# Optimization experiments

Measured on AMD Instinct MI355X. Metric: run time of the kernel, lower is better.

Reference implementation:

```python
import jax, jax.numpy as jnp
import numpy as np

N, E, DIM, H = 100000, 1600000, 128, 8
HD = DIM // H


def setup_inputs() -> dict:
    key = jax.random.key(0)
    ks = jax.random.split(key, 12)
    inp = {
        'x': jax.random.normal(ks[0], (N, DIM), dtype=jnp.float32),
        'src': jax.random.randint(ks[1], (E,), 0, N, dtype=jnp.int32),
        'dst': jax.random.randint(ks[2], (E,), 0, N, dtype=jnp.int32),
    }
    scale = 1.0 / np.sqrt(DIM)
    for i, nm in enumerate(['q', 'k', 'v', 'o']):
        inp['W' + nm] = jax.random.normal(ks[3 + 2 * i], (DIM, DIM), dtype=jnp.float32) * scale
        inp['b' + nm] = jax.random.normal(ks[4 + 2 * i], (DIM,), dtype=jnp.float32) * 0.01
    return inp


def reference(x, src, dst, Wq, bq, Wk, bk, Wv, bv, Wo, bo):
    n = x.shape[0]
    q = (x @ Wq + bq).reshape(n, H, HD)
    k = (x @ Wk + bk).reshape(n, H, HD)
    v = (x @ Wv + bv).reshape(n, H, HD)
    # per-edge score: dot(q[src], k[dst]) over head_dim  -> [E, H]
    scores = jnp.einsum('ehd,ehd->eh', q[src], k[dst]) / np.sqrt(HD).astype(np.float32)
    # edge softmax grouped by destination node
    m = jax.ops.segment_max(scores, dst, num_segments=n)        # [N, H]
    e = jnp.exp(scores - m[dst])                                 # [E, H]
    z = jax.ops.segment_sum(e, dst, num_segments=n)              # [N, H]
    attn = e / z[dst]                                            # [E, H]
    # weighted scatter-sum of source values into destinations
    agg = jax.ops.segment_sum(v[src] * attn[:, :, None], dst, num_segments=n)  # [N, H, HD]
    out = agg.reshape(n, DIM) @ Wo + bo
    return out
```

## Files before the change

### kernel.cpp

```cpp
#include <hip/hip_runtime.h>
#include <hip/hip_bf16.h>
#include <math.h>


#define CAP 64
#define CUR_STRIDE 16
#define BCHUNK 4096

typedef __attribute__((ext_vector_type(8))) short short8;
typedef __attribute__((ext_vector_type(4))) float f32x4;

__device__ inline unsigned short f2bf(float f) {
    unsigned u = __float_as_uint(f);
    unsigned r = u + 0x7fffu + ((u >> 16) & 1u);
    return (unsigned short)(r >> 16);
}
__device__ inline float bfhi2f(unsigned u) { return __uint_as_float(u & 0xffff0000u); }
__device__ inline float bflo2f(unsigned u) { return __uint_as_float(u << 16); }

__device__ inline float w_perm(const float* Wq, const float* Wk, const float* Wv,
                               int k, int c) {
    if (c < 256) {
        int g = c >> 2, r = c & 3;
        return (r < 2) ? Wq[k * 128 + 2 * g + r] : Wv[k * 128 + 2 * g + (r - 2)];
    }
    return Wk[k * 128 + (c - 256)];
}

__global__ void pack_b_kernel(const float* __restrict__ Wq, const float* __restrict__ Wk,
                              const float* __restrict__ Wv, const float* __restrict__ Wo,
                              const float* __restrict__ bq, const float* __restrict__ bk,
                              const float* __restrict__ bv,
                              short* __restrict__ BqkvP, short* __restrict__ BoP,
                              float* __restrict__ bqkv) {
    int t = blockIdx.x * 256 + threadIdx.x;
    if (t < 24 * 4 * 64 * 8) {
        int j = t & 7, l = (t >> 3) & 63, ks = (t >> 9) & 3, ct = t >> 11;
        int c = ct * 16 + (l & 15);
        int k = ks * 32 + (l >> 4) * 8 + j;
        BqkvP[t] = (short)f2bf(w_perm(Wq, Wk, Wv, k, c));
    }
    if (t < 8 * 4 * 64 * 8) {
        int j = t & 7, l = (t >> 3) & 63, ks = (t >> 9) & 3, ct = t >> 11;
        int c = ct * 16 + (l & 15);
        int k = ks * 32 + (l >> 4) * 8 + j;
        BoP[t] = (short)f2bf(Wo[k * 128 + c]);
    }
    if (t < 384) {
        float v;
        if (t < 256) {
            int g = t >> 2, r = t & 3;
            v = (r < 2) ? bq[2 * g + r] : bv[2 * g + (r - 2)];
        } else v = bk[t - 256];
        bqkv[t] = v;
    }
}

#define QKV_STRIDE 392
__global__ __launch_bounds__(256) void gemm_qkv_mfma(const float* __restrict__ A,
        const short* __restrict__ Bp, const float* __restrict__ bias,
        short* __restrict__ qv, short* __restrict__ kb, int M) {
    __shared__ short stage[4][16][QKV_STRIDE];
    int w = threadIdx.x >> 6, l = threadIdx.x & 63;
    int row0 = blockIdx.x * 64 + w * 16;
    int lr = l & 15, lk = l >> 4;

    f32x4 acc[24];
    #pragma unroll
    for (int ct = 0; ct < 24; ++ct) {
        float b = bias[ct * 16 + lr];
        acc[ct][0] = b; acc[ct][1] = b; acc[ct][2] = b; acc[ct][3] = b;
    }

    int arow = row0 + lr;
    bool rowok = arow < M;
    const float* arp = A + (size_t)arow * 128;

    #pragma unroll
    for (int ks = 0; ks < 4; ++ks) {
        f32x4 a0 = {0.f, 0.f, 0.f, 0.f}, a1 = {0.f, 0.f, 0.f, 0.f};
        if (rowok) {
            a0 = *(const f32x4*)(arp + ks * 32 + lk * 8);
            a1 = *(const f32x4*)(arp + ks * 32 + lk * 8 + 4);
        }
        short8 af;
        af[0] = (short)f2bf(a0[0]); af[1] = (short)f2bf(a0[1]);
        af[2] = (short)f2bf(a0[2]); af[3] = (short)f2bf(a0[3]);
        af[4] = (short)f2bf(a1[0]); af[5] = (short)f2bf(a1[1]);
        af[6] = (short)f2bf(a1[2]); af[7] = (short)f2bf(a1[3]);
        #pragma unroll
        for (int ct = 0; ct < 24; ++ct) {
            short8 bf = *(const short8*)(Bp + ((size_t)(ct * 4 + ks) * 64 + l) * 8);
            acc[ct] = __builtin_amdgcn_mfma_f32_16x16x32_bf16(af, bf, acc[ct], 0, 0, 0);
        }
    }

    #pragma unroll
    for (int ct = 0; ct < 24; ++ct) {
        int c = ct * 16 + lr;
        #pragma unroll
        for (int j = 0; j < 4; ++j)
            stage[w][lk * 4 + j][c] = (short)f2bf(acc[ct][j]);
    }
    __syncthreads();

    #pragma unroll
    for (int it = 0; it < 8; ++it) {
        int rr = it * 2 + (l >> 5);
        int row = row0 + rr;
        if (row < M) {
            short8 vqv = *(const short8*)&stage[w][rr][(l & 31) * 8];
            *(short8*)(qv + (size_t)row * 256 + (l & 31) * 8) = vqv;
        }
    }
    #pragma unroll
    for (int it = 0; it < 4; ++it) {
        int rr = it * 4 + (l >> 4);
        int row = row0 + rr;
        if (row < M) {
            short8 vk = *(const short8*)&stage[w][rr][256 + (l & 15) * 8];
            *(short8*)(kb + (size_t)row * 128 + (l & 15) * 8) = vk;
        }
    }
}

__global__ __launch_bounds__(256) void build_kernel(const int* __restrict__ src,
        const int* __restrict__ dst, int* __restrict__ cursor, int* __restrict__ csr,
        int E, int per8) {
    int xcd = blockIdx.x & 7;
    int chunk = blockIdx.x >> 3;
    int lo = xcd * per8, hi = lo + per8;
    int base = chunk * BCHUNK;
    #pragma unroll
    for (int it = 0; it < BCHUNK / 256; ++it) {
        int e = base + it * 256 + threadIdx.x;
        if (e < E) {
            int d = __builtin_nontemporal_load(dst + e);
            int s = __builtin_nontemporal_load(src + e);
            if (d >= lo && d < hi) {
                int slot = atomicAdd(&cursor[d << 4], 1);
                if (slot < CAP) csr[((size_t)d << 6) + slot] = s;
            }
        }
    }
}

#define EDGE_BODY(ss)                                                          \
    {                                                                          \
        uint2 u = *(const uint2*)(qv + (size_t)(ss) * 256 + l * 4);            \
        float p = bflo2f(u.x) * kdx + bfhi2f(u.x) * kdy;                       \
        p += __shfl_xor(p, 1);                                                 \
        p += __shfl_xor(p, 2);                                                 \
        p += __shfl_xor(p, 4);                                                 \
        float e = __expf(p * 0.25f);                                           \
        z += e;                                                                \
        ax += e * bflo2f(u.y);                                                 \
        ay += e * bfhi2f(u.y);                                                 \
    }

#define AGG_STRIDE 68
__global__ __launch_bounds__(256) void edge_out_kernel(const short* __restrict__ qv,
        const short* __restrict__ kb, const int* __restrict__ cursor,
        const int* __restrict__ csr, const short* __restrict__ BoP,
        const float* __restrict__ bo, float* __restrict__ out, int N, int per8) {
    __shared__ unsigned aggLds[16][AGG_STRIDE];
    int w  = threadIdx.x >> 6;
    int l  = threadIdx.x & 63;
    int lr = l & 15, lk = l >> 4;
    int xcd = blockIdx.x & 7;
    int jb  = blockIdx.x >> 3;
    int sliceN = per8 < (N - xcd * per8) ? per8 : (N - xcd * per8);
    int local0 = jb * 16;

    #pragma unroll
    for (int q = 0; q < 4; ++q) {
        int i = w * 4 + q;
        int local = local0 + i;
        if (local < sliceN) {
            int d = xcd * per8 + local;
            int deg = cursor[d << 4];
            int n = (deg < CAP) ? deg : CAP;
            const int* ep = csr + ((size_t)d << 6);
            unsigned kpk = __builtin_nontemporal_load(
                (const unsigned*)(kb + (size_t)d * 128 + 2 * l));
            float kdx = bflo2f(kpk), kdy = bfhi2f(kpk);

            float z = 0.f, ax = 0.f, ay = 0.f;
            int ii = 0;
            for (; ii + 4 <= n; ii += 4) {
                int s0 = ep[ii];
                int s1 = ep[ii + 1];
                int s2 = ep[ii + 2];
                int s3 = ep[ii + 3];
                EDGE_BODY(s0)
                EDGE_BODY(s1)
                EDGE_BODY(s2)
                EDGE_BODY(s3)
            }
            for (; ii < n; ++ii) {
                int s0 = ep[ii];
                EDGE_BODY(s0)
            }

            float zi = (z > 0.f) ? 1.0f / z : 0.f;
            aggLds[i][l] = (unsigned)f2bf(ax * zi) | ((unsigned)f2bf(ay * zi) << 16);
        }
    }
    __syncthreads();

    f32x4 acc[2];
    #pragma unroll
    for (int t = 0; t < 2; ++t) {
        float b = bo[(w * 2 + t) * 16 + lr];
        acc[t][0] = b; acc[t][1] = b; acc[t][2] = b; acc[t][3] = b;
    }

    #pragma unroll
    for (int ks = 0; ks < 4; ++ks) {
        short8 af = *(const short8*)&aggLds[lr][ks * 16 + lk * 4];
        #pragma unroll
        for (int t = 0; t < 2; ++t) {
            int ct = w * 2 + t;
            short8 bf = *(const short8*)(BoP + ((size_t)(ct * 4 + ks) * 64 + l) * 8);
            acc[t] = __builtin_amdgcn_mfma_f32_16x16x32_bf16(af, bf, acc[t], 0, 0, 0);
        }
    }

    #pragma unroll
    for (int t = 0; t < 2; ++t) {
        int c = (w * 2 + t) * 16 + lr;
        #pragma unroll
        for (int j = 0; j < 4; ++j) {
            int localr = local0 + lk * 4 + j;
            if (localr < sliceN) {
                int r = xcd * per8 + localr;
                out[(size_t)r * 128 + c] = acc[t][j];
            }
        }
    }
}

extern "C" void kernel_launch(void* const* d_in, const int* in_sizes, int n_in,
                              void* d_out, int out_size, void* d_ws, size_t ws_size,
                              hipStream_t stream) {
    const float* x   = (const float*)d_in[0];
    const int*   src = (const int*)d_in[1];
    const int*   dst = (const int*)d_in[2];
    const float* Wq  = (const float*)d_in[3];
    const float* bq  = (const float*)d_in[4];
    const float* Wk  = (const float*)d_in[5];
    const float* bk  = (const float*)d_in[6];
    const float* Wv  = (const float*)d_in[7];
    const float* bv  = (const float*)d_in[8];
    const float* Wo  = (const float*)d_in[9];
    const float* bo  = (const float*)d_in[10];
    float* out = (float*)d_out;

    int N = in_sizes[0] / 128;
    int E = in_sizes[1];
    int per8 = (N + 7) / 8;

    char* ws = (char*)d_ws;
    size_t off = 0;
    auto alloc = [&](size_t bytes) -> void* {
        void* p = ws + off;
        off = (off + bytes + 255) & ~(size_t)255;
        return p;
    };
    short* BqkvP  = (short*)alloc((size_t)24 * 4 * 64 * 8 * 2);
    short* BoP    = (short*)alloc((size_t)8 * 4 * 64 * 8 * 2);
    float* bqkv   = (float*)alloc(384 * 4);
    short* qv     = (short*)alloc((size_t)N * 256 * 2);
    short* kb     = (short*)alloc((size_t)N * 128 * 2);
    int* csr      = (int*)alloc((size_t)N * CAP * 4);
    int* cursor   = (int*)alloc((size_t)N * CUR_STRIDE * 4);
    (void)ws_size; (void)n_in; (void)out_size;

    hipMemsetAsync(cursor, 0, (size_t)N * CUR_STRIDE * 4, stream);

    pack_b_kernel<<<192, 256, 0, stream>>>(Wq, Wk, Wv, Wo, bq, bk, bv, BqkvP, BoP, bqkv);

    gemm_qkv_mfma<<<(N + 63) / 64, 256, 0, stream>>>(x, BqkvP, bqkv, qv, kb, N);

    int nchunks = (E + BCHUNK - 1) / BCHUNK;
    build_kernel<<<nchunks * 8, 256, 0, stream>>>(src, dst, cursor, csr, E, per8);

    int nb16 = (per8 + 15) / 16;
    edge_out_kernel<<<nb16 * 8, 256, 0, stream>>>(qv, kb, cursor, csr, BoP, bo, out, N, per8);
}
```

Measured before the change: 304.9 us.

## Replace 8x-redundant edge scan with two-pass binning by XCD partition

The old CSR build launched 8 copies of each edge chunk, one per XCD destination range, so src/dst were read eight times. Now a bin kernel reads each edge once and buckets (src,dst) pairs by destination partition into per-group buffers using LDS atomics and a magic-number divide. A second scatter kernel, one block per group and bucket, does the global cursor atomics. This trades the repeated edge reads for an extra write and read of the binned pairs, and it silently drops edges if a bucket exceeds CAPB.

```diff
diff --git a/kernel.cpp b/kernel.cpp
--- a/kernel.cpp
+++ b/kernel.cpp
@@ -5,7 +5,8 @@
 
 #define CAP 64
 #define CUR_STRIDE 16
-#define BCHUNK 4096
+#define GS 2048
+#define CAPB 352
 
 typedef __attribute__((ext_vector_type(8))) short short8;
 typedef __attribute__((ext_vector_type(4))) float f32x4;
@@ -124,24 +125,42 @@
     }
 }
 
-__global__ __launch_bounds__(256) void build_kernel(const int* __restrict__ src,
-        const int* __restrict__ dst, int* __restrict__ cursor, int* __restrict__ csr,
-        int E, int per8) {
-    int xcd = blockIdx.x & 7;
-    int chunk = blockIdx.x >> 3;
-    int lo = xcd * per8, hi = lo + per8;
-    int base = chunk * BCHUNK;
-    #pragma unroll
-    for (int it = 0; it < BCHUNK / 256; ++it) {
-        int e = base + it * 256 + threadIdx.x;
+__global__ __launch_bounds__(256) void bin_kernel(const int* __restrict__ src,
+        const int* __restrict__ dst, uint2* __restrict__ ebuf, int* __restrict__ bcnt,
+        int E, unsigned magic) {
+    __shared__ int cnt[8];
+    int t = threadIdx.x;
+    if (t < 8) cnt[t] = 0;
+    __syncthreads();
+    int base = blockIdx.x * GS;
+    #pragma unroll
+    for (int i = 0; i < GS / 256; ++i) {
+        int e = base + i * 256 + t;
         if (e < E) {
             int d = __builtin_nontemporal_load(dst + e);
             int s = __builtin_nontemporal_load(src + e);
-            if (d >= lo && d < hi) {
-                int slot = atomicAdd(&cursor[d << 4], 1);
-                if (slot < CAP) csr[((size_t)d << 6) + slot] = s;
-            }
-        }
+            unsigned x = (unsigned)(((unsigned long long)(unsigned)d * magic) >> 40);
+            int slot = atomicAdd(&cnt[x], 1);
+            if (slot < CAPB)
+                ebuf[((size_t)blockIdx.x * 8 + x) * CAPB + slot] =
+                    make_uint2((unsigned)s, (unsigned)d);
+        }
+    }
+    __syncthreads();
+    if (t < 8) bcnt[blockIdx.x * 8 + t] = cnt[t];
+}
+
+__global__ __launch_bounds__(256) void scatter2_kernel(const uint2* __restrict__ ebuf,
+        const int* __restrict__ bcnt, int* __restrict__ cursor, int* __restrict__ csr) {
+    int b = blockIdx.x;
+    int c = bcnt[b];
+    if (c > CAPB) c = CAPB;
+    const uint2* p = ebuf + (size_t)b * CAPB;
+    for (int i = threadIdx.x; i < c; i += 256) {
+        uint2 sd = p[i];
+        int d = (int)sd.y;
+        int slot = atomicAdd(&cursor[d << 4], 1);
+        if (slot < CAP) csr[((size_t)d << 6) + slot] = (int)sd.x;
     }
 }
 
@@ -259,6 +278,9 @@
     int N = in_sizes[0] / 128;
     int E = in_sizes[1];
     int per8 = (N + 7) / 8;
+    unsigned magic = (unsigned)(((1ull << 40) + (unsigned long long)per8 - 1) /
+                                (unsigned long long)per8);
+    int ngroups = (E + GS - 1) / GS;
 
     char* ws = (char*)d_ws;
     size_t off = 0;
@@ -274,16 +296,20 @@
     short* kb     = (short*)alloc((size_t)N * 128 * 2);
     int* csr      = (int*)alloc((size_t)N * CAP * 4);
     int* cursor   = (int*)alloc((size_t)N * CUR_STRIDE * 4);
+    uint2* ebuf   = (uint2*)alloc((size_t)ngroups * 8 * CAPB * 8);
+    int* bcnt     = (int*)alloc((size_t)ngroups * 8 * 4);
     (void)ws_size; (void)n_in; (void)out_size;
 
     hipMemsetAsync(cursor, 0, (size_t)N * CUR_STRIDE * 4, stream);
+    hipMemsetAsync(bcnt, 0, (size_t)ngroups * 8 * 4, stream);
 
     pack_b_kernel<<<192, 256, 0, stream>>>(Wq, Wk, Wv, Wo, bq, bk, bv, BqkvP, BoP, bqkv);
 
+    bin_kernel<<<ngroups, 256, 0, stream>>>(src, dst, ebuf, bcnt, E, magic);
+
     gemm_qkv_mfma<<<(N + 63) / 64, 256, 0, stream>>>(x, BqkvP, bqkv, qv, kb, N);
 
-    int nchunks = (E + BCHUNK - 1) / BCHUNK;
-    build_kernel<<<nchunks * 8, 256, 0, stream>>>(src, dst, cursor, csr, E, per8);
+    scatter2_kernel<<<ngroups * 8, 256, 0, stream>>>(ebuf, bcnt, cursor, csr);
 
     int nb16 = (per8 + 15) / 16;
     edge_out_kernel<<<nb16 * 8, 256, 0, stream>>>(qv, kb, cursor, csr, BoP, bo, out, N, per8);
```

Result: slower. 311.8 us (+2.2%).

## Process four edges per wavefront with per-lane 8-element head slices in edge kernel

Applied to the files above, without the earlier changes.

The q/v packing changes from 2-wide interleaving to 8-wide q then 8-wide v chunks per half-head, so each lane loads 32 contiguous bytes holding its q and v slice. The edge kernel splits the wavefront into 4 slots of 16 lanes, each slot handling a different edge, so four edges are gathered at once with wider loads and a single shuffle per score. Partial sums are then reduced across slots with cross-lane shuffles. The build kernel also skips loading src for edges outside the block's destination range. The aim is fewer, wider gather loads and more memory-level parallelism, paid for with extra cross-slot shuffles, inactive lanes on tail edges, and more registers.

```diff
diff --git a/kernel.cpp b/kernel.cpp
--- a/kernel.cpp
+++ b/kernel.cpp
@@ -21,8 +21,8 @@
 __device__ inline float w_perm(const float* Wq, const float* Wk, const float* Wv,
                                int k, int c) {
     if (c < 256) {
-        int g = c >> 2, r = c & 3;
-        return (r < 2) ? Wq[k * 128 + 2 * g + r] : Wv[k * 128 + 2 * g + (r - 2)];
+        int hh = c >> 4, r = c & 15;
+        return (r < 8) ? Wq[k * 128 + hh * 8 + r] : Wv[k * 128 + hh * 8 + (r - 8)];
     }
     return Wk[k * 128 + (c - 256)];
 }
@@ -49,8 +49,8 @@
     if (t < 384) {
         float v;
         if (t < 256) {
-            int g = t >> 2, r = t & 3;
-            v = (r < 2) ? bq[2 * g + r] : bv[2 * g + (r - 2)];
+            int hh = t >> 4, r = t & 15;
+            v = (r < 8) ? bq[hh * 8 + r] : bv[hh * 8 + (r - 8)];
         } else v = bk[t - 256];
         bqkv[t] = v;
     }
@@ -136,8 +136,8 @@
         int e = base + it * 256 + threadIdx.x;
         if (e < E) {
             int d = __builtin_nontemporal_load(dst + e);
-            int s = __builtin_nontemporal_load(src + e);
             if (d >= lo && d < hi) {
+                int s = __builtin_nontemporal_load(src + e);
                 int slot = atomicAdd(&cursor[d << 4], 1);
                 if (slot < CAP) csr[((size_t)d << 6) + slot] = s;
             }
@@ -145,20 +145,29 @@
     }
 }
 
-#define EDGE_BODY(ss)                                                          \
+#define AGG_STRIDE 68
+
+#define EDGE_ITER(EIDX)                                                        \
     {                                                                          \
-        uint2 u = *(const uint2*)(qv + (size_t)(ss) * 256 + l * 4);            \
-        float p = bflo2f(u.x) * kdx + bfhi2f(u.x) * kdy;                       \
+        int eidx = (EIDX);                                                     \
+        bool act = eidx < n;                                                   \
+        int s = act ? ep[eidx] : 0;                                            \
+        const uint4* qp = (const uint4*)(qv + (size_t)s * 256 + h2 * 16);      \
+        uint4 qq = qp[0];                                                      \
+        uint4 vv = qp[1];                                                      \
+        float p = bflo2f(qq.x) * kf[0] + bfhi2f(qq.x) * kf[1]                  \
+                + bflo2f(qq.y) * kf[2] + bfhi2f(qq.y) * kf[3]                  \
+                + bflo2f(qq.z) * kf[4] + bfhi2f(qq.z) * kf[5]                  \
+                + bflo2f(qq.w) * kf[6] + bfhi2f(qq.w) * kf[7];                 \
         p += __shfl_xor(p, 1);                                                 \
-        p += __shfl_xor(p, 2);                                                 \
-        p += __shfl_xor(p, 4);                                                 \
-        float e = __expf(p * 0.25f);                                           \
-        z += e;                                                                \
-        ax += e * bflo2f(u.y);                                                 \
-        ay += e * bfhi2f(u.y);                                                 \
-    }
-
-#define AGG_STRIDE 68
+        float ee = act ? __expf(p * 0.25f) : 0.f;                              \
+        z += ee;                                                               \
+        ag[0] += ee * bflo2f(vv.x); ag[1] += ee * bfhi2f(vv.x);                \
+        ag[2] += ee * bflo2f(vv.y); ag[3] += ee * bfhi2f(vv.y);                \
+        ag[4] += ee * bflo2f(vv.z); ag[5] += ee * bfhi2f(vv.z);                \
+        ag[6] += ee * bflo2f(vv.w); ag[7] += ee * bfhi2f(vv.w);                \
+    }
+
 __global__ __launch_bounds__(256) void edge_out_kernel(const short* __restrict__ qv,
         const short* __restrict__ kb, const int* __restrict__ cursor,
         const int* __restrict__ csr, const short* __restrict__ BoP,
@@ -167,6 +176,8 @@
     int w  = threadIdx.x >> 6;
     int l  = threadIdx.x & 63;
     int lr = l & 15, lk = l >> 4;
+    int h2 = l & 15;
+    int slot = l >> 4;
     int xcd = blockIdx.x & 7;
     int jb  = blockIdx.x >> 3;
     int sliceN = per8 < (N - xcd * per8) ? per8 : (N - xcd * per8);
@@ -181,29 +192,41 @@
             int deg = cursor[d << 4];
             int n = (deg < CAP) ? deg : CAP;
             const int* ep = csr + ((size_t)d << 6);
-            unsigned kpk = __builtin_nontemporal_load(
-                (const unsigned*)(kb + (size_t)d * 128 + 2 * l));
-            float kdx = bflo2f(kpk), kdy = bfhi2f(kpk);
-
-            float z = 0.f, ax = 0.f, ay = 0.f;
-            int ii = 0;
-            for (; ii + 4 <= n; ii += 4) {
-                int s0 = ep[ii];
-                int s1 = ep[ii + 1];
-                int s2 = ep[ii + 2];
-                int s3 = ep[ii + 3];
-                EDGE_BODY(s0)
-                EDGE_BODY(s1)
-                EDGE_BODY(s2)
-                EDGE_BODY(s3)
-            }
-            for (; ii < n; ++ii) {
-                int s0 = ep[ii];
-                EDGE_BODY(s0)
+
+            uint4 kk = *(const uint4*)(kb + (size_t)d * 128 + h2 * 8);
+            float kf[8];
+            kf[0] = bflo2f(kk.x); kf[1] = bfhi2f(kk.x);
+            kf[2] = bflo2f(kk.y); kf[3] = bfhi2f(kk.y);
+            kf[4] = bflo2f(kk.z); kf[5] = bfhi2f(kk.z);
+            kf[6] = bflo2f(kk.w); kf[7] = bfhi2f(kk.w);
+
+            float z = 0.f;
+            float ag[8] = {0.f, 0.f, 0.f, 0.f, 0.f, 0.f, 0.f, 0.f};
+
+            int base = 0;
+            for (; base + 8 <= n + 7; base += 8) {
+                EDGE_ITER(base + slot)
+                EDGE_ITER(base + 4 + slot)
+                if (base + 8 >= n) break;
+            }
+
+            z += __shfl_xor(z, 16);
+            z += __shfl_xor(z, 32);
+            #pragma unroll
+            for (int j = 0; j < 8; ++j) {
+                ag[j] += __shfl_xor(ag[j], 16);
+                ag[j] += __shfl_xor(ag[j], 32);
             }
 
             float zi = (z > 0.f) ? 1.0f / z : 0.f;
-            aggLds[i][l] = (unsigned)f2bf(ax * zi) | ((unsigned)f2bf(ay * zi) << 16);
+            if (slot == 0) {
+                #pragma unroll
+                for (int j = 0; j < 4; ++j) {
+                    unsigned pk = (unsigned)f2bf(ag[2 * j] * zi) |
+                                  ((unsigned)f2bf(ag[2 * j + 1] * zi) << 16);
+                    aggLds[i][h2 * 4 + j] = pk;
+                }
+            }
         }
     }
     __syncthreads();
```

Result: faster. 298.4 us (-2.1%).
